# Kernel optimization log

Hardware: AMD Instinct MI355X
Metric: run time of the kernel (lower is better)

Reference implementation:

```python
import jax, jax.numpy as jnp
import numpy as np

# Geometry constants (match init_kwargs)
PHI, T, H, W = 720, 512, 256, 256
ANGLE_RATIO = 1.0
RHO = float(np.sqrt(2.0))          # radius of detector span: ||max_pt-min_pt||/2 for [-1,1]^2
DPHI = float(np.pi) * ANGLE_RATIO / PHI   # uniform angle cell width (== mean angle step)
DT = 2.0 * RHO / T                 # detector cell width
T0 = -RHO + 0.5 * DT               # first detector cell center
DX = 2.0 / H                       # pixel width


def setup_inputs() -> dict:
    key = jax.random.key(0)
    k1, k2 = jax.random.split(key)
    sinos = jax.random.normal(k1, (32, PHI, T), dtype=jnp.float32)
    kernel = jax.random.normal(k2, (T // 2 + 1,), dtype=jnp.float32)
    return {"sinos": sinos, "kernel": kernel}


def _backproject(sino):
    """Parallel-beam backprojection (adjoint Radon), linear interp in t.

    sino: [B, PHI, T] -> image [B, H, W].
    f(x) = sum_phi g(phi, x.cos(phi)+y.sin(phi)) * dphi, zero outside detector.
    """
    angles = (jnp.arange(PHI, dtype=sino.dtype) + 0.5) * DPHI  # cell centers
    xs = (-1.0 + (jnp.arange(H, dtype=sino.dtype) + 0.5) * DX)
    X, Y = jnp.meshgrid(xs, xs, indexing='ij')  # [H, W] pixel centers

    def step(acc, inp):
        g, ang = inp                         # g: [B, T] sinogram slice at angle ang
        t = X * jnp.cos(ang) + Y * jnp.sin(ang)   # [H, W] detector coordinate
        u = (t - T0) / DT                    # fractional detector index
        i0 = jnp.floor(u)
        w = u - i0
        i0 = i0.astype(jnp.int32)
        i1 = i0 + 1
        w0 = jnp.where((i0 >= 0) & (i0 < T), 1.0 - w, 0.0)
        w1 = jnp.where((i1 >= 0) & (i1 < T), w, 0.0)
        i0c = jnp.clip(i0, 0, T - 1)
        i1c = jnp.clip(i1, 0, T - 1)
        v = g[:, i0c] * w0 + g[:, i1c] * w1  # [B, H, W]
        return acc + v, None

    B = sino.shape[0]
    acc0 = jnp.zeros((B, H, W), dtype=sino.dtype)
    sino_p = jnp.moveaxis(sino, 1, 0)        # [PHI, B, T] for scan over angles
    acc, _ = jax.lax.scan(step, acc0, (sino_p, angles))
    return acc * DPHI


def reference(sinos, kernel):
    # FFT-domain 1D filtering along detector axis, then backprojection
    filtered = jnp.fft.irfft(jnp.fft.rfft(sinos, axis=-1) * kernel, n=T, axis=-1)
    return _backproject(filtered.astype(sinos.dtype))
```

## Files before the change

### kernel.cpp

```cpp
#include <hip/hip_runtime.h>
#include <hip/hip_bf16.h>

#define NPHI 720
#define NT   512
#define NH   256
#define NB   32

#define DPHI_F   0.004363323129985824f
#define INV_DT_F 181.01933598375618f
#define DX_F     0.0078125f
#define W2PI_F   0.012271846303085130f

#define FSTR 520

typedef __fp16  h2   __attribute__((ext_vector_type(2)));
typedef _Float16 f16x2 __attribute__((ext_vector_type(2)));
typedef _Float16 f16x8 __attribute__((ext_vector_type(8)));
typedef float    f32x4 __attribute__((ext_vector_type(4)));
typedef float    f32x4u __attribute__((ext_vector_type(4), aligned(4)));
typedef float    f32x2u __attribute__((ext_vector_type(2), aligned(4)));

__device__ __forceinline__ float fdot2f(h2 a, float b_bits, float c) {
    return __builtin_amdgcn_fdot2(__builtin_bit_cast(f16x2, a),
                                  __builtin_bit_cast(f16x2, b_bits), c, false);
}

#define ASTR 40
#define BSTR 40

__global__ __launch_bounds__(512) void front_kernel(const float* __restrict__ g,
                                                    const float* __restrict__ kern,
                                                    float* __restrict__ ws,
                                                    float4* __restrict__ out4,
                                                    float* __restrict__ filt) {
    __shared__ __attribute__((aligned(16))) unsigned short As[64 * ASTR];
    __shared__ __attribute__((aligned(16))) unsigned short Bs[512 * BSTR];
    __shared__ float hloc[512];
    const int bid = (int)blockIdx.x;
    const int tid = threadIdx.x;

    if (bid < 360) {
        float* ctab = (float*)As;
        float* kkp  = (float*)Bs;
        if (tid < 257) kkp[tid] = kern[tid];
        ctab[tid] = cosf((float)tid * W2PI_F);
        __syncthreads();
        {
            float acc = 0.f;
            for (int k = 1; k < 256; ++k)
                acc += kkp[k] * ctab[(k * tid) & 511];
            hloc[tid] = (kkp[0] + ((tid & 1) ? -kkp[256] : kkp[256]) + 2.f * acc)
                        * (1.f / 512.f);
        }
        __syncthreads();
        {
            unsigned int uu[16];
            #pragma unroll
            for (int q = 0; q < 16; ++q) {
                float lo = hloc[(tid - 2 * q) & 511];
                float hi = hloc[(tid - 2 * q - 1) & 511];
                h2 p = __builtin_amdgcn_cvt_pkrtz(lo, hi);
                uu[q] = __builtin_bit_cast(unsigned int, p);
            }
            unsigned int* dst = (unsigned int*)&Bs[tid * BSTR];
            *(uint4*)(dst)      = make_uint4(uu[0], uu[1], uu[2], uu[3]);
            *(uint4*)(dst + 4)  = make_uint4(uu[4], uu[5], uu[6], uu[7]);
            *(uint4*)(dst + 8)  = make_uint4(uu[8], uu[9], uu[10], uu[11]);
            *(uint4*)(dst + 12) = make_uint4(uu[12], uu[13], uu[14], uu[15]);
        }

        const int m0 = bid * 64;
        const int w = tid >> 6, l = tid & 63;
        const int wm = (w >> 2) * 32;
        const int wn = (w & 3) * 128;
        const int fr = l & 15, g16 = l >> 4;
        const int arow = tid >> 3, aq = (tid & 7) * 4;

        f32x4 acc[2][8];
        #pragma unroll
        for (int i = 0; i < 2; ++i)
            #pragma unroll
            for (int j = 0; j < 8; ++j) acc[i][j] = (f32x4){0.f, 0.f, 0.f, 0.f};

        for (int k0 = 0; k0 < 512; k0 += 32) {
            __syncthreads();
            {
                const float* src = g + (size_t)(m0 + arow) * NT + (k0 + aq);
                float4 v = *(const float4*)src;
                h2 p0 = __builtin_amdgcn_cvt_pkrtz(v.x, v.y);
                h2 p1 = __builtin_amdgcn_cvt_pkrtz(v.z, v.w);
                *(uint2*)&As[arow * ASTR + aq] =
                    make_uint2(__builtin_bit_cast(unsigned int, p0),
                               __builtin_bit_cast(unsigned int, p1));
            }
            __syncthreads();

            f16x8 af[2], bf[8];
            #pragma unroll
            for (int i = 0; i < 2; ++i)
                af[i] = *(const f16x8*)&As[(wm + i * 16 + fr) * ASTR + g16 * 8];
            const int rbase = (wn + fr - k0) & 511;
            #pragma unroll
            for (int j = 0; j < 8; ++j) {
                const int row = (rbase + j * 16) & 511;
                bf[j] = *(const f16x8*)&Bs[row * BSTR + g16 * 8];
            }
            #pragma unroll
            for (int i = 0; i < 2; ++i)
                #pragma unroll
                for (int j = 0; j < 8; ++j)
                    acc[i][j] = __builtin_amdgcn_mfma_f32_16x16x32_f16(af[i], bf[j], acc[i][j], 0, 0, 0);
        }

        #pragma unroll
        for (int i = 0; i < 2; ++i)
            #pragma unroll
            for (int j = 0; j < 8; ++j)
                #pragma unroll
                for (int v = 0; v < 4; ++v) {
                    int row = m0 + wm + i * 16 + g16 * 4 + v;
                    int col = wn + j * 16 + fr;
                    filt[(size_t)row * FSTR + 4 + col] = acc[i][j][v];
                }
    } else if (bid < 362) {
        int p = (bid - 360) * 512 + tid;
        if (p < NPHI) {
            float ang = ((float)p + 0.5f) * DPHI_F;
            float s, c;
            sincosf(ang, &s, &c);
            float cd = c * INV_DT_F;
            float sd = s * INV_DT_F;
            ws[512 + 4 * p + 0] = cd;
            ws[512 + 4 * p + 1] = sd;
            ws[512 + 4 * p + 2] = cd * DX_F;
            ws[512 + 4 * p + 3] = sd * DX_F;
        }
    } else if (bid < 426) {
        const float4 z = make_float4(0.f, 0.f, 0.f, 0.f);
        const int nout4 = NB * NH * NH / 4;
        for (int i = (bid - 362) * 512 + tid; i < nout4; i += 64 * 512)
            out4[i] = z;
    } else {
        const float4 z = make_float4(0.f, 0.f, 0.f, 0.f);
        const int nslots = 23040 * 2;
        for (int i = (bid - 426) * 512 + tid; i < nslots; i += 64 * 512) {
            int row = i >> 1;
            float* p = filt + (size_t)row * FSTR + ((i & 1) ? 516 : 0);
            *(float4*)p = z;
        }
    }
}

#define WCHUNK 10
#define WSTR   82
#define WREG   (WCHUNK * WSTR)

__global__ __launch_bounds__(256, 6) void backproject_kernel(const float* __restrict__ filt,
                                                             const float* __restrict__ ws,
                                                             float* __restrict__ out) {
    __shared__ __attribute__((aligned(16))) float2 win[4][WREG];
    __shared__ float cstbuf[WCHUNK];

    const int tid  = threadIdx.x;
    const int bidx = (int)blockIdx.x;
    const int sixth = bidx >> 8;
    const int rem  = bidx & 255;
    const int b    = (rem >> 6) * 8;
    const int tile = rem & 63;
    const int i0 = (tile >> 3) * 32;
    const int j0 = (tile & 7) * 32;

    const float* trig = ws + 512;

    const int w  = tid >> 6;
    const int l  = tid & 63;
    const int wi = (w >> 1) * 16, wj = (w & 1) * 16;
    const int li = l >> 3, lj = l & 7;
    const int pi = i0 + wi + 2 * li;
    const int pj = j0 + wj + 2 * lj;
    const float xi = -1.f + ((float)pi + 0.5f) * DX_F;
    const float yj = -1.f + ((float)pj + 0.5f) * DX_F;

    const int sa = tid >> 4;
    const int st = tid & 15;
    const float xlo = -1.f + ((float)i0 + 0.5f) * DX_F;
    const float xhi = xlo + 31.f * DX_F;
    const float ylo = -1.f + ((float)j0 + 0.5f) * DX_F;
    const float yhi = ylo + 31.f * DX_F;

    const float* fb0 = filt + (size_t)b * (NPHI * FSTR);

    float acc[8][2][2];
    #pragma unroll
    for (int bb = 0; bb < 8; ++bb)
        #pragma unroll
        for (int di = 0; di < 2; ++di)
            #pragma unroll
            for (int dj = 0; dj < 2; ++dj) acc[bb][di][dj] = 0.f;

    const int pbeg = sixth * 120;
    for (int p0 = pbeg; p0 < pbeg + 120; p0 += WCHUNK) {
        __syncthreads();
        if (sa < WCHUNK && st < 14) {
            const int p = p0 + sa;
            const float4 tg = *(const float4*)&trig[p * 4];
            const float umin = 256.5f + fminf(xlo * tg.x, xhi * tg.x)
                                      + fminf(ylo * tg.y, yhi * tg.y);
            const float b0f = floorf(umin) - 1.f;
            if (st == 0) cstbuf[sa] = 256.5f - b0f;
            const int b0 = (int)b0f;
            const int base  = b0 + 5 * st - 1;
            const int basec = min(base, 506);
            const int s0 = sa * WSTR + (basec - b0 + 1);
            #pragma unroll
            for (int pp = 0; pp < 4; ++pp) {
                const float* rA = fb0 + (size_t)(2 * pp) * (NPHI * FSTR)
                                      + (size_t)p * FSTR + 4 + basec;
                const float* rB = rA + (size_t)(NPHI * FSTR);
                f32x4u a0 = *(const f32x4u*)rA;
                f32x2u a1 = *(const f32x2u*)(rA + 4);
                f32x4u c0 = *(const f32x4u*)rB;
                f32x2u c1 = *(const f32x2u*)(rB + 4);
                float fA[6] = {a0[0], a0[1], a0[2], a0[3], a1[0], a1[1]};
                float fB[6] = {c0[0], c0[1], c0[2], c0[3], c1[0], c1[1]};
                #pragma unroll
                for (int j = 0; j < 5; ++j) {
                    h2 pa = __builtin_amdgcn_cvt_pkrtz(fA[j], fA[j + 1]);
                    h2 pb = __builtin_amdgcn_cvt_pkrtz(fB[j], fB[j + 1]);
                    win[pp][s0 + j] = make_float2(__builtin_bit_cast(float, pa),
                                                  __builtin_bit_cast(float, pb));
                }
            }
        }
        __syncthreads();

        #pragma unroll 2
        for (int a = 0; a < WCHUNK; ++a) {
            const float4 tg = *(const float4*)&trig[(p0 + a) * 4];
            const float cst = cstbuf[a];
            const float2* wr = &win[0][a * WSTR];
            const float u00 = xi * tg.x + yj * tg.y + cst;
            #pragma unroll
            for (int di = 0; di < 2; ++di) {
                float u = di ? (u00 + tg.z) : u00;
                #pragma unroll
                for (int dj = 0; dj < 2; ++dj) {
                    float fl = floorf(u);
                    float wv = u - fl;
                    int  ip  = (int)fl;
                    h2   wp  = __builtin_amdgcn_cvt_pkrtz(1.f - wv, wv);
                    float2 s01 = wr[ip];
                    float2 s23 = wr[ip + WREG];
                    float2 s45 = wr[ip + 2 * WREG];
                    float2 s67 = wr[ip + 3 * WREG];
                    acc[0][di][dj] = fdot2f(wp, s01.x, acc[0][di][dj]);
                    acc[1][di][dj] = fdot2f(wp, s01.y, acc[1][di][dj]);
                    acc[2][di][dj] = fdot2f(wp, s23.x, acc[2][di][dj]);
                    acc[3][di][dj] = fdot2f(wp, s23.y, acc[3][di][dj]);
                    acc[4][di][dj] = fdot2f(wp, s45.x, acc[4][di][dj]);
                    acc[5][di][dj] = fdot2f(wp, s45.y, acc[5][di][dj]);
                    acc[6][di][dj] = fdot2f(wp, s67.x, acc[6][di][dj]);
                    acc[7][di][dj] = fdot2f(wp, s67.y, acc[7][di][dj]);
                    u += tg.w;
                }
            }
        }
    }

    #pragma unroll
    for (int bb = 0; bb < 8; ++bb) {
        float* ob = out + (size_t)(b + bb) * (NH * NH) + (size_t)pi * NH + pj;
        #pragma unroll
        for (int di = 0; di < 2; ++di)
            #pragma unroll
            for (int dj = 0; dj < 2; ++dj)
                unsafeAtomicAdd(ob + di * NH + dj, acc[bb][di][dj] * DPHI_F);
    }
}

extern "C" void kernel_launch(void* const* d_in, const int* in_sizes, int n_in,
                              void* d_out, int out_size, void* d_ws, size_t ws_size,
                              hipStream_t stream) {
    const float* sinos = (const float*)d_in[0];
    const float* kern  = (const float*)d_in[1];
    float* out = (float*)d_out;
    float* ws  = (float*)d_ws;

    float* filt = ws + 4096;

    hipLaunchKernelGGL(front_kernel, dim3(490), dim3(512), 0, stream,
                       sinos, kern, ws, (float4*)out, filt);
    hipLaunchKernelGGL(backproject_kernel, dim3(6 * (NB / 8) * 64), dim3(256), 0, stream,
                       filt, ws, out);
}
```

Before: 198.1 us.

## Prefetch next angle chunk into registers while computing current chunk

Restructures the staging loop to software-pipeline global loads: the filtered sinogram window for the next chunk of angles is loaded into registers before the current chunk is accumulated, then packed and written to LDS at the top of the next iteration. The chunk size drops from 10 to 8 angles, and the loading threads are remapped so each 32-thread group covers two batch pairs, putting all 256 threads to work. This is meant to hide global-load latency behind the accumulation math, at the cost of about 24 extra live registers per thread, which may reduce occupancy under the 6-blocks launch bound, and more barrier rounds per block.

```diff
diff --git a/kernel.cpp b/kernel.cpp
--- a/kernel.cpp
+++ b/kernel.cpp
@@ -151,7 +151,7 @@
     }
 }
 
-#define WCHUNK 10
+#define WCHUNK 8
 #define WSTR   82
 #define WREG   (WCHUNK * WSTR)
 
@@ -181,8 +181,11 @@
     const float xi = -1.f + ((float)pi + 0.5f) * DX_F;
     const float yj = -1.f + ((float)pj + 0.5f) * DX_F;
 
-    const int sa = tid >> 4;
-    const int st = tid & 15;
+    const int sa = tid >> 5;
+    const int sq = tid & 31;
+    const int sg = sq >> 4;
+    const int st = sq & 15;
+    const bool sact = (st < 14);
     const float xlo = -1.f + ((float)i0 + 0.5f) * DX_F;
     const float xhi = xlo + 31.f * DX_F;
     const float ylo = -1.f + ((float)j0 + 0.5f) * DX_F;
@@ -198,42 +201,63 @@
             #pragma unroll
             for (int dj = 0; dj < 2; ++dj) acc[bb][di][dj] = 0.f;
 
+    float fst[4][6];
+    float b0reg = 0.f;
+    int   s0reg = 0;
+
+    auto LOADREGS = [&](int p0c) {
+        if (!sact) return;
+        const int p = p0c + sa;
+        const float4 tg = *(const float4*)&trig[p * 4];
+        const float umin = 256.5f + fminf(xlo * tg.x, xhi * tg.x)
+                                  + fminf(ylo * tg.y, yhi * tg.y);
+        const float b0f = floorf(umin) - 1.f;
+        b0reg = b0f;
+        const int b0 = (int)b0f;
+        const int base  = b0 + 5 * st - 1;
+        const int basec = min(base, 506);
+        s0reg = sa * WSTR + (basec - b0 + 1);
+        #pragma unroll
+        for (int pr = 0; pr < 2; ++pr) {
+            const float* rA = fb0 + (size_t)(4 * sg + 2 * pr) * (NPHI * FSTR)
+                                  + (size_t)p * FSTR + 4 + basec;
+            const float* rB = rA + (size_t)(NPHI * FSTR);
+            f32x4u a0 = *(const f32x4u*)rA;
+            f32x2u a1 = *(const f32x2u*)(rA + 4);
+            f32x4u c0 = *(const f32x4u*)rB;
+            f32x2u c1 = *(const f32x2u*)(rB + 4);
+            fst[2*pr+0][0] = a0[0]; fst[2*pr+0][1] = a0[1]; fst[2*pr+0][2] = a0[2];
+            fst[2*pr+0][3] = a0[3]; fst[2*pr+0][4] = a1[0]; fst[2*pr+0][5] = a1[1];
+            fst[2*pr+1][0] = c0[0]; fst[2*pr+1][1] = c0[1]; fst[2*pr+1][2] = c0[2];
+            fst[2*pr+1][3] = c0[3]; fst[2*pr+1][4] = c1[0]; fst[2*pr+1][5] = c1[1];
+        }
+    };
+
+    auto WRITE_LDS = [&]() {
+        if (!sact) return;
+        if (st == 0 && sg == 0) cstbuf[sa] = 256.5f - b0reg;
+        #pragma unroll
+        for (int pr = 0; pr < 2; ++pr) {
+            #pragma unroll
+            for (int j = 0; j < 5; ++j) {
+                h2 pa = __builtin_amdgcn_cvt_pkrtz(fst[2*pr+0][j], fst[2*pr+0][j+1]);
+                h2 pb = __builtin_amdgcn_cvt_pkrtz(fst[2*pr+1][j], fst[2*pr+1][j+1]);
+                win[2 * sg + pr][s0reg + j] =
+                    make_float2(__builtin_bit_cast(float, pa),
+                                __builtin_bit_cast(float, pb));
+            }
+        }
+    };
+
     const int pbeg = sixth * 120;
-    for (int p0 = pbeg; p0 < pbeg + 120; p0 += WCHUNK) {
+    LOADREGS(pbeg);
+    for (int c = 0; c < 15; ++c) {
         __syncthreads();
-        if (sa < WCHUNK && st < 14) {
-            const int p = p0 + sa;
-            const float4 tg = *(const float4*)&trig[p * 4];
-            const float umin = 256.5f + fminf(xlo * tg.x, xhi * tg.x)
-                                      + fminf(ylo * tg.y, yhi * tg.y);
-            const float b0f = floorf(umin) - 1.f;
-            if (st == 0) cstbuf[sa] = 256.5f - b0f;
-            const int b0 = (int)b0f;
-            const int base  = b0 + 5 * st - 1;
-            const int basec = min(base, 506);
-            const int s0 = sa * WSTR + (basec - b0 + 1);
-            #pragma unroll
-            for (int pp = 0; pp < 4; ++pp) {
-                const float* rA = fb0 + (size_t)(2 * pp) * (NPHI * FSTR)
-                                      + (size_t)p * FSTR + 4 + basec;
-                const float* rB = rA + (size_t)(NPHI * FSTR);
-                f32x4u a0 = *(const f32x4u*)rA;
-                f32x2u a1 = *(const f32x2u*)(rA + 4);
-                f32x4u c0 = *(const f32x4u*)rB;
-                f32x2u c1 = *(const f32x2u*)(rB + 4);
-                float fA[6] = {a0[0], a0[1], a0[2], a0[3], a1[0], a1[1]};
-                float fB[6] = {c0[0], c0[1], c0[2], c0[3], c1[0], c1[1]};
-                #pragma unroll
-                for (int j = 0; j < 5; ++j) {
-                    h2 pa = __builtin_amdgcn_cvt_pkrtz(fA[j], fA[j + 1]);
-                    h2 pb = __builtin_amdgcn_cvt_pkrtz(fB[j], fB[j + 1]);
-                    win[pp][s0 + j] = make_float2(__builtin_bit_cast(float, pa),
-                                                  __builtin_bit_cast(float, pb));
-                }
-            }
-        }
+        WRITE_LDS();
         __syncthreads();
-
+        if (c + 1 < 15) LOADREGS(pbeg + (c + 1) * WCHUNK);
+
+        const int p0 = pbeg + c * WCHUNK;
         #pragma unroll 2
         for (int a = 0; a < WCHUNK; ++a) {
             const float4 tg = *(const float4*)&trig[(p0 + a) * 4];
```

After: 183.5 us (median of 2 runs). 1.08x faster.
